# Kernel optimization log

Measured on AMD Instinct MI355X. Metric: run time of the kernel, lower is better.

Reference implementation:

```python
import jax, jax.numpy as jnp
import numpy as np
from jax import lax

M = 32        # matrixSize
NMAX = 9      # color_code_number


def _conv3(x, w, b):
    # 3x3, stride 1, pad 1 (spatial-preserving), NCHW/OIHW
    y = lax.conv_general_dilated(x, w, (1, 1), ((1, 1), (1, 1)),
                                 dimension_numbers=('NCHW', 'OIHW', 'NCHW'))
    return y + b[None, :, None, None]


def _cnn(x, masks, w1, b1, w2, b2, w3, b3, fcw, fcb):
    # x: [1, C, H, W]; masks: [NM, H, W] int (binary regions)
    c = x.shape[1]
    xv = x.reshape(c, -1)                       # [C, H*W]
    feat = xv
    n = min(NMAX, masks.shape[0])
    # per-mask mean subtraction; later masks overwrite (index_copy_ semantics),
    # mean always taken from the ORIGINAL features x_view
    for i in range(n):
        m = (masks[i].reshape(-1) > 0).astype(x.dtype)
        cnt = m.sum()
        valid = cnt >= 10.0
        mean = (xv * m).sum(axis=1, keepdims=True) / jnp.maximum(cnt, 1.0)
        feat = jnp.where((m > 0) & valid, xv - mean, feat)
    f = _conv3(jax.nn.relu(_conv3(jax.nn.relu(_conv3(feat.reshape(x.shape), w1, b1)), w2, b2)), w3, b3)
    fv = f.reshape(f.shape[1], -1)              # [M, H*W]
    mats, valids = [], []
    for i in range(n):
        m = (masks[i].reshape(-1) == 1).astype(x.dtype)
        cnt = m.sum()
        sel = fv * m                            # masked gather as multiply
        cov = (sel @ sel.T) / jnp.maximum(cnt, 1.0)   # [M, M]
        mats.append(fcw @ cov.reshape(-1) + fcb)      # fc on flattened cov
        valids.append(cnt >= 10.0)
    return jnp.stack(mats), jnp.stack(valids), feat


def _forward(cF, sF, cmasks, smasks, sp, cp, compress_w, compress_b, unzip_w, unzip_b):
    sMats, svalid, _ = _cnn(sF, smasks, *sp)
    cMats, cvalid, cF_sub = _cnn(cF, cmasks, *cp)
    ccv = compress_w @ cF_sub + compress_b[:, None]   # 1x1 conv -> [M, H*W]
    trans = ccv
    sFF = sF.reshape(sF.shape[1], -1)                 # [C, H*W]
    finalSMean = jnp.zeros((cF.shape[1], cF.shape[2] * cF.shape[3]), cF.dtype)
    n = min(NMAX, cmasks.shape[0], smasks.shape[0])
    for i in range(n):
        cm = (cmasks[i].reshape(-1) == 1).astype(cF.dtype)
        sm = (smasks[i].reshape(-1) == 1).astype(cF.dtype)
        valid = (cm.sum() >= 10.0) & (sm.sum() >= 10.0) & svalid[i] & cvalid[i]
        sMean = (sFF * sm).sum(axis=1, keepdims=True) / jnp.maximum(sm.sum(), 1.0)
        tm = sMats[i].reshape(M, M) @ cMats[i].reshape(M, M)
        trans = jnp.where((cm > 0) & valid, tm @ ccv, trans)
        finalSMean = jnp.where((cm > 0) & valid, sMean, finalSMean)
    out = (unzip_w @ trans + unzip_b[:, None]).reshape(cF.shape)  # 1x1 unzip
    return out + finalSMean.reshape(cF.shape)


def setup_inputs() -> dict:
    key = jax.random.key(0)
    ks = jax.random.split(key, 32)
    H = W = 256
    C = 512
    NM = 4

    def p(k, shape, s=0.05):
        return jax.random.normal(k, shape, jnp.float32) * s

    inp = {
        'cF': jax.random.normal(ks[0], (1, C, H, W), jnp.float32),
        'sF': jax.random.normal(ks[1], (1, C, H, W), jnp.float32),
        'cmasks': jax.random.randint(ks[2], (NM, H, W), 0, 2, jnp.int32),
        'smasks': jax.random.randint(ks[3], (NM, H, W), 0, 2, jnp.int32),
        # snet CNN (r41): 512->256->128->32, fc 1024->1024
        'snet_w1': p(ks[4], (256, 512, 3, 3)), 'snet_b1': jnp.zeros(256, jnp.float32),
        'snet_w2': p(ks[5], (128, 256, 3, 3)), 'snet_b2': jnp.zeros(128, jnp.float32),
        'snet_w3': p(ks[6], (M, 128, 3, 3)), 'snet_b3': jnp.zeros(M, jnp.float32),
        'snet_fcw': p(ks[7], (M * M, M * M)), 'snet_fcb': jnp.zeros(M * M, jnp.float32),
        # cnet CNN
        'cnet_w1': p(ks[8], (256, 512, 3, 3)), 'cnet_b1': jnp.zeros(256, jnp.float32),
        'cnet_w2': p(ks[9], (128, 256, 3, 3)), 'cnet_b2': jnp.zeros(128, jnp.float32),
        'cnet_w3': p(ks[10], (M, 128, 3, 3)), 'cnet_b3': jnp.zeros(M, jnp.float32),
        'cnet_fcw': p(ks[11], (M * M, M * M)), 'cnet_fcb': jnp.zeros(M * M, jnp.float32),
        # compress / unzip 1x1 convs as [O, I] matmuls
        'compress_w': p(ks[12], (M, C)), 'compress_b': jnp.zeros(M, jnp.float32),
        'unzip_w': p(ks[13], (C, M)), 'unzip_b': jnp.zeros(C, jnp.float32),
    }
    return inp


def reference(cF, sF, cmasks, smasks,
              snet_w1, snet_b1, snet_w2, snet_b2, snet_w3, snet_b3, snet_fcw, snet_fcb,
              cnet_w1, cnet_b1, cnet_w2, cnet_b2, cnet_w3, cnet_b3, cnet_fcw, cnet_fcb,
              compress_w, compress_b, unzip_w, unzip_b):
    sp = (snet_w1, snet_b1, snet_w2, snet_b2, snet_w3, snet_b3, snet_fcw, snet_fcb)
    cp = (cnet_w1, cnet_b1, cnet_w2, cnet_b2, cnet_w3, cnet_b3, cnet_fcw, cnet_fcb)
    return _forward(cF, sF, cmasks, smasks, sp, cp, compress_w, compress_b, unzip_w, unzip_b)
```

## Files before the change

### kernel.cpp

```cpp
#include <hip/hip_runtime.h>

#define HDIM 256
#define WDIM 256
#define HW   65536
#define CDIM 512

using bf16x8 = __attribute__((ext_vector_type(8))) short;
using f32x4  = __attribute__((ext_vector_type(4))) float;

__device__ __forceinline__ unsigned short f2bf(float f) {
    unsigned u = __builtin_bit_cast(unsigned, f);
    u += 0x7FFFu + ((u >> 16) & 1u);
    return (unsigned short)(u >> 16);
}

__device__ __forceinline__ void gload_lds16(const void* g, void* l) {
    __builtin_amdgcn_global_load_lds((const __attribute__((address_space(1))) unsigned int*)g,
                                     (__attribute__((address_space(3))) unsigned int*)l, 16, 0, 0);
}


__global__ __launch_bounds__(256) void zero_small_k(int* __restrict__ cnt,
                                                    float* __restrict__ covraw,
                                                    float* __restrict__ zp) {
    int t = blockIdx.x * 256 + threadIdx.x;
    if (t < 8) cnt[t] = 0;
    if (t < 8192) covraw[t] = 0.f;
    if (t < 64) zp[t] = 0.f;
}

__global__ __launch_bounds__(256) void pack_masks_k(const int* __restrict__ cm,
                                                    const int* __restrict__ sm,
                                                    int n,
                                                    unsigned char* __restrict__ ccode,
                                                    unsigned char* __restrict__ scode,
                                                    int* __restrict__ cnt) {
    int p = blockIdx.x * 256 + threadIdx.x;
    unsigned cc = 0, sc = 0;
    for (int i = 0; i < n; ++i) {
        if (cm[i * HW + p] != 0) cc |= (1u << i);
        if (sm[i * HW + p] != 0) sc |= (1u << i);
    }
    ccode[p] = (unsigned char)cc;
    scode[p] = (unsigned char)sc;
    int lane = threadIdx.x & 63;
    for (int i = 0; i < n; ++i) {
        unsigned long long bc = __ballot((cc >> i) & 1);
        unsigned long long bs = __ballot((sc >> i) & 1);
        if (lane == 0) {
            atomicAdd(&cnt[i],     (int)__popcll(bc));
            atomicAdd(&cnt[4 + i], (int)__popcll(bs));
        }
    }
}

__global__ __launch_bounds__(256) void masked_means_k(const float* __restrict__ cF,
                                                      const float* __restrict__ sF,
                                                      const unsigned char* __restrict__ ccode,
                                                      const unsigned char* __restrict__ scode,
                                                      const int* __restrict__ cnt,
                                                      float* __restrict__ cmean5,
                                                      float* __restrict__ smean5) {
    int b = blockIdx.x;
    const float* x; const unsigned char* code; const int* cn; float* mout;
    if (b < CDIM) { x = cF; code = ccode; cn = cnt;     mout = cmean5; }
    else          { x = sF; code = scode; cn = cnt + 4; mout = smean5; b -= CDIM; }
    const int c = b;
    const int t = threadIdx.x;
    const float4* x4 = (const float4*)(x + (size_t)c * HW);
    const unsigned* cd4 = (const unsigned*)code;
    float s0 = 0.f, s1 = 0.f, s2 = 0.f, s3 = 0.f;
    for (int i = t; i < HW / 4; i += 256) {
        float4 v = x4[i];
        unsigned cd = cd4[i];
        float vv;
        vv = v.x;
        if (cd & 0x01u) s0 += vv;
        if (cd & 0x02u) s1 += vv;
        if (cd & 0x04u) s2 += vv;
        if (cd & 0x08u) s3 += vv;
        vv = v.y;
        if (cd & 0x0100u) s0 += vv;
        if (cd & 0x0200u) s1 += vv;
        if (cd & 0x0400u) s2 += vv;
        if (cd & 0x0800u) s3 += vv;
        vv = v.z;
        if (cd & 0x010000u) s0 += vv;
        if (cd & 0x020000u) s1 += vv;
        if (cd & 0x040000u) s2 += vv;
        if (cd & 0x080000u) s3 += vv;
        vv = v.w;
        if (cd & 0x01000000u) s0 += vv;
        if (cd & 0x02000000u) s1 += vv;
        if (cd & 0x04000000u) s2 += vv;
        if (cd & 0x08000000u) s3 += vv;
    }
    __shared__ float red[4][256];
    red[0][t] = s0; red[1][t] = s1; red[2][t] = s2; red[3][t] = s3;
    __syncthreads();
    for (int off = 128; off; off >>= 1) {
        if (t < off) {
            red[0][t] += red[0][t + off];
            red[1][t] += red[1][t + off];
            red[2][t] += red[2][t + off];
            red[3][t] += red[3][t + off];
        }
        __syncthreads();
    }
    if (t < 4) mout[t * CDIM + c] = red[t][0] / fmaxf((float)cn[t], 1.f);
    if (t == 4) mout[4 * CDIM + c] = 0.f;
}

__global__ __launch_bounds__(256) void idx_maps_k(const unsigned char* __restrict__ ccode,
                                                  const unsigned char* __restrict__ scode,
                                                  const int* __restrict__ cnt, int n,
                                                  signed char* __restrict__ cidx,
                                                  signed char* __restrict__ sidx,
                                                  signed char* __restrict__ fidx) {
    int p = blockIdx.x * 256 + threadIdx.x;
    int cc = ccode[p], sc = scode[p];
    int ci = 4, si = 4, fi = 4;
    for (int i = 0; i < n; ++i) {
        bool cv = cnt[i] >= 10;
        bool sv = cnt[4 + i] >= 10;
        if (((cc >> i) & 1) && cv) ci = i;
        if (((sc >> i) & 1) && sv) si = i;
        if (((cc >> i) & 1) && cv && sv) fi = i;
    }
    cidx[p] = (signed char)ci;
    sidx[p] = (signed char)si;
    fidx[p] = (signed char)fi;
}


__global__ __launch_bounds__(256) void wtrans_k(const float* __restrict__ w,
                                                unsigned short* __restrict__ wt,
                                                int COUT, int CIN) {
    int t = blockIdx.x * 256 + threadIdx.x;
    int total = COUT * CIN * 9;
    if (t >= total) return;
    int oc = t / (CIN * 9);
    int rem = t - oc * (CIN * 9);
    int ci = rem / 9;
    int tap = rem - ci * 9;
    wt[(size_t)(((ci >> 5) * 9 + tap) * COUT + oc) * 32 + (ci & 31)] = f2bf(w[t]);
}

__global__ __launch_bounds__(256) void wctrans_k(const float* __restrict__ w,
                                                 unsigned short* __restrict__ wc) {
    int t = blockIdx.x * 256 + threadIdx.x;
    if (t >= 32 * 512) return;
    int oc = t >> 9, ci = t & 511;
    wc[(size_t)((ci >> 5) * 32 + oc) * 32 + (ci & 31)] = f2bf(w[t]);
}

__global__ __launch_bounds__(256) void trans_in_k(const float* __restrict__ X,
                                                  const float* __restrict__ mean5,
                                                  const signed char* __restrict__ idx5,
                                                  unsigned short* __restrict__ Xt) {
    __shared__ unsigned s32[64 * 33];
    const int tid = threadIdx.x;
    const int p0 = blockIdx.x * 64;
    const int c0 = blockIdx.y * 64;
    const int cpair = tid >> 3;
    const int q = tid & 7;
    const int ch0 = c0 + cpair * 2;
    const float* X0 = X + (size_t)ch0 * HW;
    const float* X1 = X0 + HW;
#pragma unroll
    for (int k = 0; k < 2; ++k) {
        int px0 = (q + k * 8) * 4;
        float4 va = *(const float4*)(X0 + p0 + px0);
        float4 vb = *(const float4*)(X1 + p0 + px0);
        int id4 = *(const int*)(idx5 + p0 + px0);
        float a[4] = {va.x, va.y, va.z, va.w};
        float b[4] = {vb.x, vb.y, vb.z, vb.w};
#pragma unroll
        for (int j = 0; j < 4; ++j) {
            int id = (id4 >> (8 * j)) & 0xFF;
            const float* mr = mean5 + id * CDIM;
            unsigned u = (unsigned)f2bf(a[j] - mr[ch0])
                       | ((unsigned)f2bf(b[j] - mr[ch0 + 1]) << 16);
            s32[(px0 + j) * 33 + cpair] = u;
        }
    }
    __syncthreads();
    const int px = tid >> 2, h = tid & 3;
    const unsigned* rp = &s32[px * 33 + h * 8];
    uint4 u0 = *(const uint4*)(rp);
    uint4 u1 = *(const uint4*)(rp + 4);
    unsigned short* dst = Xt + (size_t)(p0 + px) * CDIM + c0 + h * 16;
    *(uint4*)dst = u0;
    *(uint4*)(dst + 8) = u1;
}

template <int CIN, int COUT, int BM, int BN, bool RELU>
__global__ __launch_bounds__(256, 2) void convmf2_k(const unsigned short* __restrict__ Xt,
                                                    const unsigned short* __restrict__ Wt,
                                                    const float* __restrict__ bias,
                                                    unsigned short* __restrict__ Yt,
                                                    const unsigned short* __restrict__ zp) {
    constexpr int WM = BM / 4;
    constexpr int FM = WM / 16;
    constexpr int FN = BN / 16;
    constexpr int PXT = BN + 2;
    constexpr int PXTP = BN + 6;
    constexpr int NCH = 12 * PXTP;
    constexpr int NCHP = (NCH + 255) & ~255;
    constexpr int NCB = CIN / 32;
    constexpr int TPR = WDIM / BN;
    constexpr int NBX = HDIM * TPR;
    constexpr int PER = NBX / 8;
    __shared__ unsigned short s_tile[2][NCHP * 8];

    const int tid = threadIdx.x;
    const int ln = tid & 63, wid = tid >> 6;
    const int ln15 = ln & 15, g = ln >> 4;

    const int b = blockIdx.x;
    const int xcd = b & 7;
    const int k = b >> 3;
    const int xt = xcd * PER + (k % PER);
    const int yt = k / PER;

    const int y0 = xt / TPR;
    const int x0 = (xt % TPR) * BN;
    const int ocb = yt * BM;

    auto stage = [&](int buf, int cb) {
#pragma unroll
        for (int c0 = 0; c0 < NCH; c0 += 256) {
            int c = c0 + tid;
            if (c < NCH) {
                int grow = c / PXTP;
                int px = c - grow * PXTP;
                int ky = grow >> 2, gg = grow & 3;
                int y = y0 + ky - 1;
                int x = x0 - 1 + px;
                bool ok = (px < PXT) && ((unsigned)y < HDIM) && ((unsigned)x < WDIM);
                const unsigned short* src = ok
                    ? Xt + (size_t)(y * WDIM + x) * CIN + cb * 32 + gg * 8
                    : zp;
                gload_lds16(src, &s_tile[buf][(size_t)(c0 + wid * 64) * 8]);
            }
        }
    };

    f32x4 acc[FM][FN];
#pragma unroll
    for (int i = 0; i < FM; ++i)
#pragma unroll
        for (int j = 0; j < FN; ++j) acc[i][j] = f32x4{0.f, 0.f, 0.f, 0.f};

    const unsigned short* wfb = Wt + (size_t)(ocb + wid * WM + ln15) * 32 + g * 8;

    stage(0, 0);

    for (int cb = 0; cb < NCB; ++cb) {
        const int buf = cb & 1;
        __syncthreads();
        bf16x8 wreg[9][FM];
#pragma unroll
        for (int tap = 0; tap < 9; ++tap)
#pragma unroll
            for (int mf = 0; mf < FM; ++mf)
                wreg[tap][mf] = *(const bf16x8*)(wfb + (size_t)((cb * 9 + tap) * COUT + mf * 16) * 32);
        if (cb + 1 < NCB) stage(buf ^ 1, cb + 1);
        const unsigned short* st = &s_tile[buf][0];
#pragma unroll
        for (int tap = 0; tap < 9; ++tap) {
            const int ky = tap / 3, kx = tap - ky * 3;
            bf16x8 bfr[FN];
#pragma unroll
            for (int nf = 0; nf < FN; ++nf) {
                int slot = (ky * 4 + g) * PXTP + kx + nf * 16 + ln15;
                bfr[nf] = *(const bf16x8*)&st[(size_t)slot * 8];
            }
#pragma unroll
            for (int mf = 0; mf < FM; ++mf)
#pragma unroll
                for (int nf = 0; nf < FN; ++nf)
                    acc[mf][nf] = __builtin_amdgcn_mfma_f32_16x16x32_bf16(wreg[tap][mf], bfr[nf], acc[mf][nf], 0, 0, 0);
        }
    }

    const int p0 = y0 * WDIM + x0;
#pragma unroll
    for (int nf = 0; nf < FN; ++nf) {
        const size_t p = (size_t)p0 + nf * 16 + ln15;
#pragma unroll
        for (int mf = 0; mf < FM; ++mf) {
            const int oc0 = ocb + wid * WM + mf * 16 + g * 4;
            const float4 bi = *(const float4*)(bias + oc0);
            f32x4 v = acc[mf][nf];
            float r0 = v[0] + bi.x, r1 = v[1] + bi.y, r2 = v[2] + bi.z, r3 = v[3] + bi.w;
            if (RELU) {
                r0 = fmaxf(r0, 0.f); r1 = fmaxf(r1, 0.f);
                r2 = fmaxf(r2, 0.f); r3 = fmaxf(r3, 0.f);
            }
            unsigned lo = (unsigned)f2bf(r0) | ((unsigned)f2bf(r1) << 16);
            unsigned hi = (unsigned)f2bf(r2) | ((unsigned)f2bf(r3) << 16);
            *(uint2*)(Yt + p * COUT + oc0) = uint2{lo, hi};
        }
    }
}

template <int CIN, int COUT, int BM, int BN, int WM, int WN, bool RELU>
__global__ __launch_bounds__(256, 2) void convmf_k(const unsigned short* __restrict__ Xt,
                                                   const unsigned short* __restrict__ Wt,
                                                   const float* __restrict__ bias,
                                                   float* __restrict__ Yf,
                                                   const unsigned short* __restrict__ zp) {
    constexpr int WAVES_N = BN / WN;
    constexpr int FM = WM / 16, FN = WN / 16;
    constexpr int PXT = BN + 2;
    constexpr int PXTP = BN + 6;
    constexpr int NCH = 12 * PXTP;
    constexpr int NCHP = (NCH + 255) & ~255;
    __shared__ unsigned short s_tile[NCHP * 8];

    const int tid = threadIdx.x;
    const int ln = tid & 63, wid = tid >> 6;
    const int ln15 = ln & 15, g = ln >> 4;
    const int wm_i = wid / WAVES_N, wn_i = wid % WAVES_N;

    const int per = gridDim.x >> 3;
    const int tile = (blockIdx.x & 7) * per + (blockIdx.x >> 3);

    constexpr int TPR = WDIM / BN;
    const int y0 = tile / TPR;
    const int x0 = (tile % TPR) * BN;
    const int ocb = blockIdx.y * BM;

    f32x4 acc[FM][FN];
#pragma unroll
    for (int i = 0; i < FM; ++i)
#pragma unroll
        for (int j = 0; j < FN; ++j) acc[i][j] = f32x4{0.f, 0.f, 0.f, 0.f};

    const unsigned short* wfb = Wt + (size_t)(ocb + wm_i * WM + ln15) * 32 + g * 8;

    for (int cb = 0; cb < CIN / 32; ++cb) {
        __syncthreads();
        for (int c0 = 0; c0 < NCH; c0 += 256) {
            int c = c0 + tid;
            if (c < NCH) {
                int grow = c / PXTP;
                int px = c - grow * PXTP;
                int ky = grow >> 2, gg = grow & 3;
                int y = y0 + ky - 1;
                int x = x0 - 1 + px;
                bool ok = (px < PXT) && ((unsigned)y < HDIM) && ((unsigned)x < WDIM);
                const unsigned short* src = ok
                    ? Xt + (size_t)(y * WDIM + x) * CIN + cb * 32 + gg * 8
                    : zp;
                gload_lds16(src, &s_tile[(size_t)(c0 + wid * 64) * 8]);
            }
        }
        bf16x8 wreg[9][FM];
#pragma unroll
        for (int tap = 0; tap < 9; ++tap)
#pragma unroll
            for (int mf = 0; mf < FM; ++mf)
                wreg[tap][mf] = *(const bf16x8*)(wfb + (size_t)((cb * 9 + tap) * COUT + mf * 16) * 32);
        __syncthreads();
#pragma unroll
        for (int tap = 0; tap < 9; ++tap) {
            const int ky = tap / 3, kx = tap - ky * 3;
            bf16x8 b[FN];
#pragma unroll
            for (int nf = 0; nf < FN; ++nf) {
                int slot = (ky * 4 + g) * PXTP + kx + wn_i * WN + nf * 16 + ln15;
                b[nf] = *(const bf16x8*)&s_tile[(size_t)slot * 8];
            }
#pragma unroll
            for (int mf = 0; mf < FM; ++mf)
#pragma unroll
                for (int nf = 0; nf < FN; ++nf)
                    acc[mf][nf] = __builtin_amdgcn_mfma_f32_16x16x32_bf16(wreg[tap][mf], b[nf], acc[mf][nf], 0, 0, 0);
        }
    }

    const int p0 = y0 * WDIM + x0;
#pragma unroll
    for (int nf = 0; nf < FN; ++nf) {
        const size_t p = (size_t)p0 + wn_i * WN + nf * 16 + ln15;
#pragma unroll
        for (int mf = 0; mf < FM; ++mf) {
            const int oc0 = ocb + wm_i * WM + mf * 16 + g * 4;
            const float4 bi = *(const float4*)(bias + oc0);
            f32x4 v = acc[mf][nf];
            float r0 = v[0] + bi.x, r1 = v[1] + bi.y, r2 = v[2] + bi.z, r3 = v[3] + bi.w;
            if (RELU) {
                r0 = fmaxf(r0, 0.f); r1 = fmaxf(r1, 0.f);
                r2 = fmaxf(r2, 0.f); r3 = fmaxf(r3, 0.f);
            }
            Yf[(size_t)(oc0 + 0) * HW + p] = r0;
            Yf[(size_t)(oc0 + 1) * HW + p] = r1;
            Yf[(size_t)(oc0 + 2) * HW + p] = r2;
            Yf[(size_t)(oc0 + 3) * HW + p] = r3;
        }
    }
}

__global__ __launch_bounds__(256, 2) void ccv_gemm_k(const unsigned short* __restrict__ Xt,
                                                     const unsigned short* __restrict__ wc,
                                                     const float* __restrict__ cbias,
                                                     float* __restrict__ ccv) {
    __shared__ unsigned short s_t[1024 * 8];
    const int tid = threadIdx.x;
    const int ln = tid & 63, wid = tid >> 6;
    const int ln15 = ln & 15, g = ln >> 4;
    const int per = gridDim.x >> 3;
    const int tile = (blockIdx.x & 7) * per + (blockIdx.x >> 3);
    const int p0 = tile * 256;

    f32x4 acc[2][4];
#pragma unroll
    for (int i = 0; i < 2; ++i)
#pragma unroll
        for (int j = 0; j < 4; ++j) acc[i][j] = f32x4{0.f, 0.f, 0.f, 0.f};

    for (int cb = 0; cb < 16; ++cb) {
        __syncthreads();
#pragma unroll
        for (int pass = 0; pass < 4; ++pass) {
            int c = pass * 256 + tid;
            int gg = c >> 8, px = c & 255;
            const unsigned short* src = Xt + (size_t)(p0 + px) * CDIM + cb * 32 + gg * 8;
            gload_lds16(src, &s_t[(size_t)c * 8]);
        }
        bf16x8 a[2];
#pragma unroll
        for (int mf = 0; mf < 2; ++mf)
            a[mf] = *(const bf16x8*)(wc + (size_t)((cb * 32 + mf * 16 + ln15) * 32) + g * 8);
        __syncthreads();
        bf16x8 b[4];
#pragma unroll
        for (int nf = 0; nf < 4; ++nf) {
            int slot = g * 256 + wid * 64 + nf * 16 + ln15;
            b[nf] = *(const bf16x8*)&s_t[(size_t)slot * 8];
        }
#pragma unroll
        for (int mf = 0; mf < 2; ++mf)
#pragma unroll
            for (int nf = 0; nf < 4; ++nf)
                acc[mf][nf] = __builtin_amdgcn_mfma_f32_16x16x32_bf16(a[mf], b[nf], acc[mf][nf], 0, 0, 0);
    }
#pragma unroll
    for (int nf = 0; nf < 4; ++nf) {
        const size_t p = (size_t)p0 + wid * 64 + nf * 16 + ln15;
#pragma unroll
        for (int mf = 0; mf < 2; ++mf) {
            const int oc0 = mf * 16 + g * 4;
            const float4 bi = *(const float4*)(cbias + oc0);
            f32x4 v = acc[mf][nf];
            ccv[(size_t)(oc0 + 0) * HW + p] = v[0] + bi.x;
            ccv[(size_t)(oc0 + 1) * HW + p] = v[1] + bi.y;
            ccv[(size_t)(oc0 + 2) * HW + p] = v[2] + bi.z;
            ccv[(size_t)(oc0 + 3) * HW + p] = v[3] + bi.w;
        }
    }
}


__global__ __launch_bounds__(256) void cov_accum_k(const float* __restrict__ f,
                                                   const unsigned char* __restrict__ code,
                                                   float* __restrict__ covraw) {
    constexpr int PCH = 256;
    __shared__ float s_f[32][PCH + 1];
    const int i = blockIdx.y;
    const int p0 = blockIdx.x * PCH;
    const int t = threadIdx.x;
    for (int e = t; e < 32 * PCH; e += 256) {
        int row = e >> 8, col = e & (PCH - 1);
        int p = p0 + col;
        float m = ((code[p] >> i) & 1u) ? 1.f : 0.f;
        s_f[row][col] = f[(size_t)row * HW + p] * m;
    }
    __syncthreads();
    const int a = t >> 3;
    const int b0 = (t & 7) * 4;
    float a0 = 0.f, a1 = 0.f, a2 = 0.f, a3 = 0.f;
    for (int p = 0; p < PCH; ++p) {
        float va = s_f[a][p];
        a0 = fmaf(va, s_f[b0 + 0][p], a0);
        a1 = fmaf(va, s_f[b0 + 1][p], a1);
        a2 = fmaf(va, s_f[b0 + 2][p], a2);
        a3 = fmaf(va, s_f[b0 + 3][p], a3);
    }
    float* dst = covraw + i * 1024 + a * 32 + b0;
    atomicAdd(dst + 0, a0);
    atomicAdd(dst + 1, a1);
    atomicAdd(dst + 2, a2);
    atomicAdd(dst + 3, a3);
}

__global__ __launch_bounds__(256) void fc_k(const float* __restrict__ fcw,
                                            const float* __restrict__ fcb,
                                            const float* __restrict__ covraw,
                                            const int* __restrict__ cnt,
                                            float* __restrict__ mats) {
    const int i = blockIdx.y;
    const int wv = threadIdx.x >> 6;
    const int lane = threadIdx.x & 63;
    const int r = blockIdx.x * 4 + wv;
    const float inv = 1.f / fmaxf((float)cnt[i], 1.f);
    float acc = 0.f;
    for (int q = lane; q < 1024; q += 64)
        acc = fmaf(fcw[r * 1024 + q], covraw[i * 1024 + q] * inv, acc);
    for (int off = 32; off; off >>= 1) acc += __shfl_down(acc, off);
    if (lane == 0) mats[i * 1024 + r] = acc + fcb[r];
}

__global__ __launch_bounds__(256) void prep_small_k(const float* __restrict__ sMats,
                                                    const float* __restrict__ cMats,
                                                    const float* __restrict__ unzip_b,
                                                    const float* __restrict__ smean5,
                                                    int n,
                                                    float* __restrict__ tm5,
                                                    float* __restrict__ B5) {
    int t = blockIdx.x * 256 + threadIdx.x;
    if (t < 5 * 1024) {
        int i = t >> 10, rc = t & 1023, r = rc >> 5, c = rc & 31;
        float v;
        if (i < n) {
            float s = 0.f;
            for (int k = 0; k < 32; ++k)
                s = fmaf(sMats[i * 1024 + r * 32 + k], cMats[i * 1024 + k * 32 + c], s);
            v = s;
        } else {
            v = (r == c) ? 1.f : 0.f;
        }
        tm5[t] = v;
    } else if (t < 5 * 1024 + 5 * 512) {
        int u = t - 5 * 1024;
        int i = u >> 9, c = u & 511;
        B5[u] = unzip_b[c] + smean5[i * CDIM + c];
    }
}

__global__ __launch_bounds__(256) void final_k(const float* __restrict__ ccv,
                                               const signed char* __restrict__ fidx,
                                               const float* __restrict__ tm5,
                                               const float* __restrict__ B5,
                                               const float* __restrict__ uw,
                                               float* __restrict__ out) {
    __shared__ float s_tm[5 * 1032];
    __shared__ float s_B[5 * 520];
    const int t = threadIdx.x;
    for (int e = t; e < 5 * 1024; e += 256) {
        int i = e >> 10, rc = e & 1023;
        s_tm[i * 1032 + rc] = tm5[e];
    }
    for (int e = t; e < 5 * 512; e += 256) {
        int i = e >> 9, c = e & 511;
        s_B[i * 520 + c] = B5[e];
    }
    __syncthreads();
    const int p = blockIdx.x * 256 + t;
    const int id = fidx[p];
    float v[32];
#pragma unroll
    for (int k = 0; k < 32; ++k) v[k] = ccv[(size_t)k * HW + p];
    float tv[32];
#pragma unroll
    for (int r = 0; r < 32; ++r) {
        float s = 0.f;
#pragma unroll
        for (int k = 0; k < 32; ++k)
            s = fmaf(s_tm[id * 1032 + r * 32 + k], v[k], s);
        tv[r] = s;
    }
    for (int c = 0; c < CDIM; ++c) {
        float s = s_B[id * 520 + c];
#pragma unroll
        for (int k = 0; k < 32; ++k)
            s = fmaf(uw[c * 32 + k], tv[k], s);
        out[(size_t)c * HW + p] = s;
    }
}


extern "C" void kernel_launch(void* const* d_in, const int* in_sizes, int n_in,
                              void* d_out, int out_size, void* d_ws, size_t ws_size,
                              hipStream_t stream) {
    const float* cF = (const float*)d_in[0];
    const float* sF = (const float*)d_in[1];
    const int* cmasks = (const int*)d_in[2];
    const int* smasks = (const int*)d_in[3];
    const float* snet_w1 = (const float*)d_in[4];
    const float* snet_b1 = (const float*)d_in[5];
    const float* snet_w2 = (const float*)d_in[6];
    const float* snet_b2 = (const float*)d_in[7];
    const float* snet_w3 = (const float*)d_in[8];
    const float* snet_b3 = (const float*)d_in[9];
    const float* snet_fcw = (const float*)d_in[10];
    const float* snet_fcb = (const float*)d_in[11];
    const float* cnet_w1 = (const float*)d_in[12];
    const float* cnet_b1 = (const float*)d_in[13];
    const float* cnet_w2 = (const float*)d_in[14];
    const float* cnet_b2 = (const float*)d_in[15];
    const float* cnet_w3 = (const float*)d_in[16];
    const float* cnet_b3 = (const float*)d_in[17];
    const float* cnet_fcw = (const float*)d_in[18];
    const float* cnet_fcb = (const float*)d_in[19];
    const float* compress_w = (const float*)d_in[20];
    const float* compress_b = (const float*)d_in[21];
    const float* unzip_w = (const float*)d_in[22];
    const float* unzip_b = (const float*)d_in[23];
    float* out = (float*)d_out;

    int nmC = in_sizes[2] / HW;
    int nmS = in_sizes[3] / HW;
    int n = nmC < nmS ? nmC : nmS;
    if (n > 4) n = 4;

    char* ws = (char*)d_ws;
    size_t off = 0;
    auto alloc = [&](size_t bytes) {
        size_t o = off;
        off += (bytes + 255) & ~(size_t)255;
        return o;
    };
    char* regA = ws + alloc((size_t)HW * 512 * 2);
    char* regB = ws + alloc((size_t)HW * 256 * 2);
    float* ccv  = (float*)(ws + alloc((size_t)32 * HW * 4));
    unsigned short* Wt1 = (unsigned short*)(ws + alloc((size_t)9 * 256 * 512 * 2));
    unsigned short* Wt2 = (unsigned short*)(ws + alloc((size_t)9 * 128 * 256 * 2));
    unsigned short* Wt3 = (unsigned short*)(ws + alloc((size_t)9 * 32 * 128 * 2));
    unsigned short* Wc  = (unsigned short*)(ws + alloc((size_t)32 * 512 * 2));
    unsigned char* ccode = (unsigned char*)(ws + alloc(HW));
    unsigned char* scode = (unsigned char*)(ws + alloc(HW));
    signed char* cidx = (signed char*)(ws + alloc(HW));
    signed char* sidx = (signed char*)(ws + alloc(HW));
    signed char* fidx = (signed char*)(ws + alloc(HW));
    int*   cnt    = (int*)(ws + alloc(8 * 4));
    float* cmean5 = (float*)(ws + alloc(5 * CDIM * 4));
    float* smean5 = (float*)(ws + alloc(5 * CDIM * 4));
    float* covraw = (float*)(ws + alloc(8 * 1024 * 4));
    float* sMats  = (float*)(ws + alloc(4 * 1024 * 4));
    float* cMats  = (float*)(ws + alloc(4 * 1024 * 4));
    float* tm5    = (float*)(ws + alloc(5 * 1024 * 4));
    float* B5     = (float*)(ws + alloc(5 * 512 * 4));
    float* zpf    = (float*)(ws + alloc(256));
    (void)ws_size; (void)n_in; (void)out_size;

    unsigned short* Xt = (unsigned short*)regA;
    unsigned short* Y2 = (unsigned short*)regA;
    unsigned short* Y1 = (unsigned short*)regB;
    float*          fbuf = (float*)regB;
    const unsigned short* zp = (const unsigned short*)zpf;

    zero_small_k<<<32, 256, 0, stream>>>(cnt, covraw, zpf);
    pack_masks_k<<<HW / 256, 256, 0, stream>>>(cmasks, smasks, n, ccode, scode, cnt);
    masked_means_k<<<2 * CDIM, 256, 0, stream>>>(cF, sF, ccode, scode, cnt, cmean5, smean5);
    idx_maps_k<<<HW / 256, 256, 0, stream>>>(ccode, scode, cnt, n, cidx, sidx, fidx);
    wctrans_k<<<(32 * 512 + 255) / 256, 256, 0, stream>>>(compress_w, Wc);

    wtrans_k<<<(9 * 256 * 512 + 255) / 256, 256, 0, stream>>>(snet_w1, Wt1, 256, 512);
    wtrans_k<<<(9 * 128 * 256 + 255) / 256, 256, 0, stream>>>(snet_w2, Wt2, 128, 256);
    wtrans_k<<<(9 * 32 * 128 + 255) / 256, 256, 0, stream>>>(snet_w3, Wt3, 32, 128);
    trans_in_k<<<dim3(HW / 64, 8), 256, 0, stream>>>(sF, smean5, sidx, Xt);
    convmf2_k<512, 256, 128, 128, true ><<<1024, 256, 0, stream>>>(Xt, Wt1, snet_b1, Y1, zp);
    convmf2_k<256, 128, 128, 128, true ><<<512, 256, 0, stream>>>(Y1, Wt2, snet_b2, Y2, zp);
    convmf_k<128, 32,  32,  256, 32, 64, false><<<dim3(256, 1), 256, 0, stream>>>(Y2, Wt3, snet_b3, fbuf, zp);
    cov_accum_k<<<dim3(HW / 256, n), 256, 0, stream>>>(fbuf, scode, covraw);
    fc_k<<<dim3(256, n), 256, 0, stream>>>(snet_fcw, snet_fcb, covraw, cnt + 4, sMats);

    wtrans_k<<<(9 * 256 * 512 + 255) / 256, 256, 0, stream>>>(cnet_w1, Wt1, 256, 512);
    wtrans_k<<<(9 * 128 * 256 + 255) / 256, 256, 0, stream>>>(cnet_w2, Wt2, 128, 256);
    wtrans_k<<<(9 * 32 * 128 + 255) / 256, 256, 0, stream>>>(cnet_w3, Wt3, 32, 128);
    trans_in_k<<<dim3(HW / 64, 8), 256, 0, stream>>>(cF, cmean5, cidx, Xt);
    ccv_gemm_k<<<HW / 256, 256, 0, stream>>>(Xt, Wc, compress_b, ccv);
    convmf2_k<512, 256, 128, 128, true ><<<1024, 256, 0, stream>>>(Xt, Wt1, cnet_b1, Y1, zp);
    convmf2_k<256, 128, 128, 128, true ><<<512, 256, 0, stream>>>(Y1, Wt2, cnet_b2, Y2, zp);
    convmf_k<128, 32,  32,  256, 32, 64, false><<<dim3(256, 1), 256, 0, stream>>>(Y2, Wt3, cnet_b3, fbuf, zp);
    cov_accum_k<<<dim3(HW / 256, n), 256, 0, stream>>>(fbuf, ccode, covraw + 4 * 1024);
    fc_k<<<dim3(256, n), 256, 0, stream>>>(cnet_fcw, cnet_fcb, covraw + 4 * 1024, cnt, cMats);

    prep_small_k<<<30, 256, 0, stream>>>(sMats, cMats, unzip_b, smean5, n, tm5, B5);
    final_k<<<HW / 256, 256, 0, stream>>>(ccv, fidx, tm5, B5, unzip_w, out);
}
```

Measured before the change: 987.2 us.

## Merge weight transforms into one prep kernel and raise conv occupancy

Folds the zero-init, compress-weight transform and all six conv weight transforms into a single launch, and gives snet and cnet separate weight buffers so no re-transform sits between the two networks. The convmf2 LDS tile padding is trimmed (PXTP from BN+6 to BN+2, with a small tail pad) and launch bounds go from 2 to 3 blocks per CU to allow higher occupancy. The tighter register budget may cause spills in the MFMA loop. The staging guard now runs per wave with a per-lane bound check.

```diff
diff --git a/kernel.cpp b/kernel.cpp
--- a/kernel.cpp
+++ b/kernel.cpp
@@ -20,14 +20,53 @@
 }
 
 
-__global__ __launch_bounds__(256) void zero_small_k(int* __restrict__ cnt,
-                                                    float* __restrict__ covraw,
-                                                    float* __restrict__ zp) {
+__device__ __forceinline__ void wtrans_one(const float* __restrict__ w,
+                                           unsigned short* __restrict__ wt,
+                                           int COUT, int CIN, int t) {
+    int oc = t / (CIN * 9);
+    int rem = t - oc * (CIN * 9);
+    int ci = rem / 9;
+    int tap = rem - ci * 9;
+    wt[(size_t)(((ci >> 5) * 9 + tap) * COUT + oc) * 32 + (ci & 31)] = f2bf(w[t]);
+}
+
+__global__ __launch_bounds__(256) void prep_all_k(int* __restrict__ cnt,
+                                                  float* __restrict__ covraw,
+                                                  float* __restrict__ zp,
+                                                  const float* __restrict__ cw, unsigned short* __restrict__ wc,
+                                                  const float* __restrict__ s1, unsigned short* __restrict__ W1s,
+                                                  const float* __restrict__ s2, unsigned short* __restrict__ W2s,
+                                                  const float* __restrict__ s3, unsigned short* __restrict__ W3s,
+                                                  const float* __restrict__ c1, unsigned short* __restrict__ W1c,
+                                                  const float* __restrict__ c2, unsigned short* __restrict__ W2c,
+                                                  const float* __restrict__ c3, unsigned short* __restrict__ W3c) {
     int t = blockIdx.x * 256 + threadIdx.x;
-    if (t < 8) cnt[t] = 0;
-    if (t < 8192) covraw[t] = 0.f;
-    if (t < 64) zp[t] = 0.f;
-}
+    if (t < 8264) {
+        if (t < 8) cnt[t] = 0;
+        else if (t < 8200) covraw[t - 8] = 0.f;
+        else if (t < 8264) zp[t - 8200] = 0.f;
+        return;
+    }
+    t -= 8264;
+    if (t < 16384) {
+        int oc = t >> 9, ci = t & 511;
+        wc[(size_t)((ci >> 5) * 32 + oc) * 32 + (ci & 31)] = f2bf(cw[t]);
+        return;
+    }
+    t -= 16384;
+    if (t < 1179648) { wtrans_one(s1, W1s, 256, 512, t); return; }
+    t -= 1179648;
+    if (t < 294912)  { wtrans_one(s2, W2s, 128, 256, t); return; }
+    t -= 294912;
+    if (t < 36864)   { wtrans_one(s3, W3s, 32, 128, t); return; }
+    t -= 36864;
+    if (t < 1179648) { wtrans_one(c1, W1c, 256, 512, t); return; }
+    t -= 1179648;
+    if (t < 294912)  { wtrans_one(c2, W2c, 128, 256, t); return; }
+    t -= 294912;
+    if (t < 36864)   { wtrans_one(c3, W3c, 32, 128, t); return; }
+}
+
 
 __global__ __launch_bounds__(256) void pack_masks_k(const int* __restrict__ cm,
                                                     const int* __restrict__ sm,
@@ -132,28 +171,6 @@
     fidx[p] = (signed char)fi;
 }
 
-
-__global__ __launch_bounds__(256) void wtrans_k(const float* __restrict__ w,
-                                                unsigned short* __restrict__ wt,
-                                                int COUT, int CIN) {
-    int t = blockIdx.x * 256 + threadIdx.x;
-    int total = COUT * CIN * 9;
-    if (t >= total) return;
-    int oc = t / (CIN * 9);
-    int rem = t - oc * (CIN * 9);
-    int ci = rem / 9;
-    int tap = rem - ci * 9;
-    wt[(size_t)(((ci >> 5) * 9 + tap) * COUT + oc) * 32 + (ci & 31)] = f2bf(w[t]);
-}
-
-__global__ __launch_bounds__(256) void wctrans_k(const float* __restrict__ w,
-                                                 unsigned short* __restrict__ wc) {
-    int t = blockIdx.x * 256 + threadIdx.x;
-    if (t >= 32 * 512) return;
-    int oc = t >> 9, ci = t & 511;
-    wc[(size_t)((ci >> 5) * 32 + oc) * 32 + (ci & 31)] = f2bf(w[t]);
-}
-
 __global__ __launch_bounds__(256) void trans_in_k(const float* __restrict__ X,
                                                   const float* __restrict__ mean5,
                                                   const signed char* __restrict__ idx5,
@@ -195,7 +212,7 @@
 }
 
 template <int CIN, int COUT, int BM, int BN, bool RELU>
-__global__ __launch_bounds__(256, 2) void convmf2_k(const unsigned short* __restrict__ Xt,
+__global__ __launch_bounds__(256, 3) void convmf2_k(const unsigned short* __restrict__ Xt,
                                                     const unsigned short* __restrict__ Wt,
                                                     const float* __restrict__ bias,
                                                     unsigned short* __restrict__ Yt,
@@ -204,14 +221,13 @@
     constexpr int FM = WM / 16;
     constexpr int FN = BN / 16;
     constexpr int PXT = BN + 2;
-    constexpr int PXTP = BN + 6;
+    constexpr int PXTP = BN + 2;
     constexpr int NCH = 12 * PXTP;
-    constexpr int NCHP = (NCH + 255) & ~255;
     constexpr int NCB = CIN / 32;
     constexpr int TPR = WDIM / BN;
     constexpr int NBX = HDIM * TPR;
     constexpr int PER = NBX / 8;
-    __shared__ unsigned short s_tile[2][NCHP * 8];
+    __shared__ unsigned short s_tile[2][NCH * 8 + 512];
 
     const int tid = threadIdx.x;
     const int ln = tid & 63, wid = tid >> 6;
@@ -230,18 +246,20 @@
     auto stage = [&](int buf, int cb) {
 #pragma unroll
         for (int c0 = 0; c0 < NCH; c0 += 256) {
-            int c = c0 + tid;
-            if (c < NCH) {
+            if (c0 + wid * 64 < NCH) {
+                int c = c0 + tid;
                 int grow = c / PXTP;
                 int px = c - grow * PXTP;
                 int ky = grow >> 2, gg = grow & 3;
                 int y = y0 + ky - 1;
                 int x = x0 - 1 + px;
-                bool ok = (px < PXT) && ((unsigned)y < HDIM) && ((unsigned)x < WDIM);
-                const unsigned short* src = ok
-                    ? Xt + (size_t)(y * WDIM + x) * CIN + cb * 32 + gg * 8
-                    : zp;
-                gload_lds16(src, &s_tile[buf][(size_t)(c0 + wid * 64) * 8]);
+                bool ok = (c < NCH) && (px < PXT) && ((unsigned)y < HDIM) && ((unsigned)x < WDIM);
+                if (c < NCH) {
+                    const unsigned short* src = ok
+                        ? Xt + (size_t)(y * WDIM + x) * CIN + cb * 32 + gg * 8
+                        : zp;
+                    gload_lds16(src, &s_tile[buf][(size_t)(c0 + wid * 64) * 8]);
+                }
             }
         }
     };
@@ -626,9 +644,12 @@
     char* regA = ws + alloc((size_t)HW * 512 * 2);
     char* regB = ws + alloc((size_t)HW * 256 * 2);
     float* ccv  = (float*)(ws + alloc((size_t)32 * HW * 4));
-    unsigned short* Wt1 = (unsigned short*)(ws + alloc((size_t)9 * 256 * 512 * 2));
-    unsigned short* Wt2 = (unsigned short*)(ws + alloc((size_t)9 * 128 * 256 * 2));
-    unsigned short* Wt3 = (unsigned short*)(ws + alloc((size_t)9 * 32 * 128 * 2));
+    unsigned short* Wt1s = (unsigned short*)(ws + alloc((size_t)9 * 256 * 512 * 2));
+    unsigned short* Wt2s = (unsigned short*)(ws + alloc((size_t)9 * 128 * 256 * 2));
+    unsigned short* Wt3s = (unsigned short*)(ws + alloc((size_t)9 * 32 * 128 * 2));
+    unsigned short* Wt1c = (unsigned short*)(ws + alloc((size_t)9 * 256 * 512 * 2));
+    unsigned short* Wt2c = (unsigned short*)(ws + alloc((size_t)9 * 128 * 256 * 2));
+    unsigned short* Wt3c = (unsigned short*)(ws + alloc((size_t)9 * 32 * 128 * 2));
     unsigned short* Wc  = (unsigned short*)(ws + alloc((size_t)32 * 512 * 2));
     unsigned char* ccode = (unsigned char*)(ws + alloc(HW));
     unsigned char* scode = (unsigned char*)(ws + alloc(HW));
@@ -652,30 +673,25 @@
     float*          fbuf = (float*)regB;
     const unsigned short* zp = (const unsigned short*)zpf;
 
-    zero_small_k<<<32, 256, 0, stream>>>(cnt, covraw, zpf);
+    prep_all_k<<<11905, 256, 0, stream>>>(cnt, covraw, zpf, compress_w, Wc,
+                                          snet_w1, Wt1s, snet_w2, Wt2s, snet_w3, Wt3s,
+                                          cnet_w1, Wt1c, cnet_w2, Wt2c, cnet_w3, Wt3c);
     pack_masks_k<<<HW / 256, 256, 0, stream>>>(cmasks, smasks, n, ccode, scode, cnt);
     masked_means_k<<<2 * CDIM, 256, 0, stream>>>(cF, sF, ccode, scode, cnt, cmean5, smean5);
     idx_maps_k<<<HW / 256, 256, 0, stream>>>(ccode, scode, cnt, n, cidx, sidx, fidx);
-    wctrans_k<<<(32 * 512 + 255) / 256, 256, 0, stream>>>(compress_w, Wc);
-
-    wtrans_k<<<(9 * 256 * 512 + 255) / 256, 256, 0, stream>>>(snet_w1, Wt1, 256, 512);
-    wtrans_k<<<(9 * 128 * 256 + 255) / 256, 256, 0, stream>>>(snet_w2, Wt2, 128, 256);
-    wtrans_k<<<(9 * 32 * 128 + 255) / 256, 256, 0, stream>>>(snet_w3, Wt3, 32, 128);
+
     trans_in_k<<<dim3(HW / 64, 8), 256, 0, stream>>>(sF, smean5, sidx, Xt);
-    convmf2_k<512, 256, 128, 128, true ><<<1024, 256, 0, stream>>>(Xt, Wt1, snet_b1, Y1, zp);
-    convmf2_k<256, 128, 128, 128, true ><<<512, 256, 0, stream>>>(Y1, Wt2, snet_b2, Y2, zp);
-    convmf_k<128, 32,  32,  256, 32, 64, false><<<dim3(256, 1), 256, 0, stream>>>(Y2, Wt3, snet_b3, fbuf, zp);
+    convmf2_k<512, 256, 128, 128, true ><<<1024, 256, 0, stream>>>(Xt, Wt1s, snet_b1, Y1, zp);
+    convmf2_k<256, 128, 128, 128, true ><<<512, 256, 0, stream>>>(Y1, Wt2s, snet_b2, Y2, zp);
+    convmf_k<128, 32,  32,  256, 32, 64, false><<<dim3(256, 1), 256, 0, stream>>>(Y2, Wt3s, snet_b3, fbuf, zp);
     cov_accum_k<<<dim3(HW / 256, n), 256, 0, stream>>>(fbuf, scode, covraw);
     fc_k<<<dim3(256, n), 256, 0, stream>>>(snet_fcw, snet_fcb, covraw, cnt + 4, sMats);
 
-    wtrans_k<<<(9 * 256 * 512 + 255) / 256, 256, 0, stream>>>(cnet_w1, Wt1, 256, 512);
-    wtrans_k<<<(9 * 128 * 256 + 255) / 256, 256, 0, stream>>>(cnet_w2, Wt2, 128, 256);
-    wtrans_k<<<(9 * 32 * 128 + 255) / 256, 256, 0, stream>>>(cnet_w3, Wt3, 32, 128);
     trans_in_k<<<dim3(HW / 64, 8), 256, 0, stream>>>(cF, cmean5, cidx, Xt);
     ccv_gemm_k<<<HW / 256, 256, 0, stream>>>(Xt, Wc, compress_b, ccv);
-    convmf2_k<512, 256, 128, 128, true ><<<1024, 256, 0, stream>>>(Xt, Wt1, cnet_b1, Y1, zp);
-    convmf2_k<256, 128, 128, 128, true ><<<512, 256, 0, stream>>>(Y1, Wt2, cnet_b2, Y2, zp);
-    convmf_k<128, 32,  32,  256, 32, 64, false><<<dim3(256, 1), 256, 0, stream>>>(Y2, Wt3, cnet_b3, fbuf, zp);
+    convmf2_k<512, 256, 128, 128, true ><<<1024, 256, 0, stream>>>(Xt, Wt1c, cnet_b1, Y1, zp);
+    convmf2_k<256, 128, 128, 128, true ><<<512, 256, 0, stream>>>(Y1, Wt2c, cnet_b2, Y2, zp);
+    convmf_k<128, 32,  32,  256, 32, 64, false><<<dim3(256, 1), 256, 0, stream>>>(Y2, Wt3c, cnet_b3, fbuf, zp);
     cov_accum_k<<<dim3(HW / 256, n), 256, 0, stream>>>(fbuf, ccode, covraw + 4 * 1024);
     fc_k<<<dim3(256, n), 256, 0, stream>>>(cnet_fcw, cnet_fcb, covraw + 4 * 1024, cnt, cMats);
 
```

Result: slower. 1.244 ms (+26.0%).
